# Kernel optimization log

Hardware: AMD Instinct MI355X
Metric: run time of the kernel (lower is better)

Reference implementation:

```python
import jax, jax.numpy as jnp
import numpy as np

N = 20000
E = 160000
H = 8          # heads
D = 96         # head_dim (768 // 8)
C = H * D      # 768 hidden channels
G = 256        # num graphs
NUM_CLASSES = 32
SLOPE = 0.2    # GATv2 LeakyReLU negative slope


def layer_norm(x, w, b, eps=1e-5):
    mu = jnp.mean(x, axis=-1, keepdims=True)
    var = jnp.mean(jnp.square(x - mu), axis=-1, keepdims=True)
    return (x - mu) * jax.lax.rsqrt(var + eps) * w + b


def gatv2_layer(x, src, dst, Wl, bl, Wr, br, att, bias):
    # x: [N, C]; src/dst: [E'] with self loops included
    xl = (x @ Wl + bl).reshape(N, H, D)   # source projection
    xr = (x @ Wr + br).reshape(N, H, D)   # target projection
    e = xl[src] + xr[dst]                 # [E', H, D] edge gather
    e = jnp.where(e > 0, e, SLOPE * e)    # LeakyReLU
    logits = jnp.einsum('ehd,hd->eh', e, att)  # [E', H]
    m = jax.ops.segment_max(logits, dst, num_segments=N)
    ex = jnp.exp(logits - m[dst])
    s = jax.ops.segment_sum(ex, dst, num_segments=N)
    alpha = ex / s[dst]                   # segment softmax over in-edges
    out = jax.ops.segment_sum(alpha[:, :, None] * xl[src], dst, num_segments=N)
    return out.reshape(N, C) + bias


def setup_inputs() -> dict:
    key = jax.random.key(0)
    ks = jax.random.split(key, 24)
    x = jax.random.normal(ks[0], (N, 768), jnp.float32)
    edge_index = jax.random.randint(ks[1], (2, E), 0, N, jnp.int64)
    batch = jnp.sort(jax.random.randint(ks[2], (N,), 0, G, jnp.int64))
    sc = 1.0 / np.sqrt(C)
    p = {
        'x': x, 'edge_index': edge_index, 'batch': batch,
        'w_in': jax.random.normal(ks[3], (768, C), jnp.float32) * sc,
        'b_in': jnp.zeros((C,), jnp.float32),
        'Wl': jax.random.normal(ks[4], (3, C, C), jnp.float32) * sc,
        'bl': jnp.zeros((3, C), jnp.float32),
        'Wr': jax.random.normal(ks[5], (3, C, C), jnp.float32) * sc,
        'br': jnp.zeros((3, C), jnp.float32),
        'att': jax.random.normal(ks[6], (3, H, D), jnp.float32) * (1.0 / np.sqrt(D)),
        'gat_bias': jnp.zeros((3, C), jnp.float32),
        'ln_w': jnp.ones((3, C), jnp.float32),
        'ln_b': jnp.zeros((3, C), jnp.float32),
        'out_ln_w': jnp.ones((3 * C,), jnp.float32),
        'out_ln_b': jnp.zeros((3 * C,), jnp.float32),
        'w_out': jax.random.normal(ks[7], (3 * C, NUM_CLASSES), jnp.float32) * (1.0 / np.sqrt(3 * C)),
        'b_out': jnp.zeros((NUM_CLASSES,), jnp.float32),
    }
    return p


def reference(x, edge_index, batch, w_in, b_in, Wl, bl, Wr, br, att, gat_bias,
              ln_w, ln_b, out_ln_w, out_ln_b, w_out, b_out):
    # add self loops (PyG add_self_loops=True)
    loops = jnp.arange(N, dtype=edge_index.dtype)
    src = jnp.concatenate([edge_index[0], loops])
    dst = jnp.concatenate([edge_index[1], loops])

    h = x @ w_in + b_in
    jumps = []
    for l in range(3):
        a = gatv2_layer(h, src, dst, Wl[l], bl[l], Wr[l], br[l], att[l], gat_bias[l])
        h = layer_norm(a + h, ln_w[l], ln_b[l])
        h = jax.nn.gelu(h, approximate=False)
        jumps.append(h)
    hc = jnp.concatenate(jumps, axis=-1)  # JumpingKnowledge 'cat' -> [N, 3C]

    # global mean pool over graphs
    sums = jax.ops.segment_sum(hc, batch, num_segments=G)
    cnt = jax.ops.segment_sum(jnp.ones((N, 1), hc.dtype), batch, num_segments=G)
    pooled = sums / jnp.maximum(cnt, 1.0)

    out = layer_norm(pooled, out_ln_w, out_ln_b)
    return out @ w_out + b_out
```

## Files before the change

### kernel.cpp

```cpp
#include <hip/hip_runtime.h>

#define N_NODES 20000
#define N_EDGES 160000
#define CH      768
#define CH3     2304
#define NGRAPH  256
#define NCLS    32

typedef __bf16 bf16v8 __attribute__((ext_vector_type(8)));
typedef float  f32x4  __attribute__((ext_vector_type(4)));

__device__ __forceinline__ float b2f(ushort u) {
    union { float f; unsigned u; } x; x.u = ((unsigned)u) << 16; return x.f;
}
__device__ __forceinline__ ushort f2b(float f) {
    union { float f; unsigned u; } x; x.f = f;
    unsigned r = x.u + 0x7FFFu + ((x.u >> 16) & 1u);
    return (ushort)(r >> 16);
}
__device__ __forceinline__ void load12(const ushort* __restrict__ p, float* o) {
    const ushort4* q = (const ushort4*)p;
    ushort4 a = q[0], b = q[1], c = q[2];
    o[0]=b2f(a.x); o[1]=b2f(a.y); o[2]=b2f(a.z); o[3]=b2f(a.w);
    o[4]=b2f(b.x); o[5]=b2f(b.y); o[6]=b2f(b.z); o[7]=b2f(b.w);
    o[8]=b2f(c.x); o[9]=b2f(c.y); o[10]=b2f(c.z); o[11]=b2f(c.w);
}
__device__ __forceinline__ void load12f(const float* __restrict__ p, float* o) {
    const float4* q = (const float4*)p;
    float4 a = q[0], b = q[1], c = q[2];
    o[0]=a.x; o[1]=a.y; o[2]=a.z; o[3]=a.w;
    o[4]=b.x; o[5]=b.y; o[6]=b.z; o[7]=b.w;
    o[8]=c.x; o[9]=c.y; o[10]=c.z; o[11]=c.w;
}
__device__ __forceinline__ void async_copy16(void* lds, const void* gp) {
    __builtin_amdgcn_global_load_lds((const void __attribute__((address_space(1)))*)gp,
                                     (void __attribute__((address_space(3)))*)lds, 16, 0, 0);
}

__global__ void cvt_x_kernel(const float* __restrict__ src, ushort* __restrict__ dst, int n4) {
    int i = blockIdx.x * 256 + threadIdx.x;
    if (i >= n4) return;
    float4 v = ((const float4*)src)[i];
    ushort4 o; o.x = f2b(v.x); o.y = f2b(v.y); o.z = f2b(v.z); o.w = f2b(v.w);
    ((ushort4*)dst)[i] = o;
}

__global__ void transpose_cvt_all(const float* __restrict__ w_in,
                                  const float* __restrict__ Wl,
                                  const float* __restrict__ Wr,
                                  ushort* __restrict__ wt_in,
                                  ushort* __restrict__ wt_l) {
    __shared__ float tile[32][33];
    int z = blockIdx.z;
    const float* in;
    ushort* out;
    if (z == 0) { in = w_in; out = wt_in; }
    else {
        int l = (z - 1) >> 1, isr = (z - 1) & 1;
        in  = (isr ? Wr : Wl) + (size_t)l * CH * CH;
        out = wt_l + (size_t)l * 1536 * CH + (size_t)isr * CH * CH;
    }
    int bx = blockIdx.x * 32, by = blockIdx.y * 32;
    int tx = threadIdx.x, ty = threadIdx.y;
    #pragma unroll
    for (int i = ty; i < 32; i += 8) tile[i][tx] = in[(size_t)(by + i) * CH + bx + tx];
    __syncthreads();
    #pragma unroll
    for (int i = ty; i < 32; i += 8) out[(size_t)(bx + i) * CH + by + tx] = f2b(tile[tx][i]);
}

__global__ void init_kernel(int* deg, int* gcount, int n) {
    int i = blockIdx.x * 256 + threadIdx.x;
    if (i < n) deg[i] = 1;
    if (i < 256) gcount[i] = 0;
}
__global__ void count_both_kernel(const int* __restrict__ dst, int* __restrict__ deg, int e,
                                  const int* __restrict__ batch, int* __restrict__ gcount, int n) {
    int i = blockIdx.x * 256 + threadIdx.x;
    if (i < e) atomicAdd(&deg[dst[i]], 1);
    if (i < n) atomicAdd(&gcount[batch[i]], 1);
}
__global__ __launch_bounds__(1024) void scan_kernel(const int* __restrict__ deg,
                                                    int* __restrict__ rowptr, int n) {
    __shared__ int part[1024];
    int t = threadIdx.x;
    const int chunk = (n + 1023) / 1024;
    int base = t * chunk;
    int s = 0;
    for (int i = 0; i < chunk; ++i) { int idx = base + i; if (idx < n) s += deg[idx]; }
    part[t] = s; __syncthreads();
    for (int off = 1; off < 1024; off <<= 1) {
        int v = (t >= off) ? part[t - off] : 0;
        __syncthreads();
        part[t] += v;
        __syncthreads();
    }
    int run = (t == 0) ? 0 : part[t - 1];
    for (int i = 0; i < chunk; ++i) {
        int idx = base + i;
        if (idx < n) { rowptr[idx] = run; run += deg[idx]; }
    }
    if (t == 1023) rowptr[n] = part[1023];
}
__global__ void selfloop_kernel(const int* __restrict__ rowptr, int* __restrict__ csrc,
                                int* __restrict__ cursor, int n) {
    int i = blockIdx.x * 256 + threadIdx.x;
    if (i < n) { int p = rowptr[i]; csrc[p] = i; cursor[i] = p + 1; }
}
__global__ void scatter_kernel(const int* __restrict__ src, const int* __restrict__ dst,
                               int* __restrict__ cursor, int* __restrict__ csrc, int e) {
    int i = blockIdx.x * 256 + threadIdx.x;
    if (i < e) { int p = atomicAdd(&cursor[dst[i]], 1); csrc[p] = src[i]; }
}
__global__ __launch_bounds__(256) void gscan_kernel(const int* __restrict__ gcount,
                                                    int* __restrict__ gstart) {
    __shared__ int p[256];
    int t = threadIdx.x;
    p[t] = gcount[t]; __syncthreads();
    for (int off = 1; off < 256; off <<= 1) {
        int v = (t >= off) ? p[t - off] : 0;
        __syncthreads();
        p[t] += v;
        __syncthreads();
    }
    gstart[t] = p[t] - gcount[t];
    if (t == 255) gstart[256] = p[255];
}

__global__ __launch_bounds__(256) void gemm_bf16_kernel(
    const ushort* __restrict__ A, int lda,
    const ushort* __restrict__ Bt,
    const float* __restrict__ biasA, const float* __restrict__ biasB, int nsplit,
    ushort* __restrict__ C, int ldc, int M) {
    __shared__ __bf16 As[128 * 32];
    __shared__ __bf16 Bs[128 * 32];
    int tid = threadIdx.x;
    int wave = tid >> 6, lane = tid & 63;
    int wr = wave >> 1, wc = wave & 1;

    int bid = blockIdx.y * gridDim.x + blockIdx.x;
    int pf = 8 * gridDim.y;
    int p  = bid / pf;
    int rem = bid - p * pf;
    int rp = min(8, (int)gridDim.x - p * 8);
    int row_t = p * 8 + rem % rp;
    int col_t = rem / rp;
    int row0 = row_t * 128, col0 = col_t * 128;

    int c1 = wave * 64 + lane, c2 = c1 + 256;
    int ar1 = min(row0 + (c1 >> 2), M - 1), ak1 = (c1 & 3) * 8;
    int ar2 = min(row0 + (c2 >> 2), M - 1), ak2 = (c2 & 3) * 8;
    int br1 = col0 + (c1 >> 2), br2 = col0 + (c2 >> 2);
    const ushort* a1 = A + (size_t)ar1 * lda + ak1;
    const ushort* a2 = A + (size_t)ar2 * lda + ak2;
    const ushort* b1 = Bt + (size_t)br1 * CH + ak1;
    const ushort* b2 = Bt + (size_t)br2 * CH + ak2;
    __bf16* asb1 = As + (wave * 64) * 8;
    __bf16* asb2 = As + (256 + wave * 64) * 8;
    __bf16* bsb1 = Bs + (wave * 64) * 8;
    __bf16* bsb2 = Bs + (256 + wave * 64) * 8;

    f32x4 acc[4][4] = {};
    int l16 = lane & 15, lq = lane >> 4;

    for (int k0 = 0; k0 < CH; k0 += 32) {
        async_copy16(asb1, a1 + k0);
        async_copy16(asb2, a2 + k0);
        async_copy16(bsb1, b1 + k0);
        async_copy16(bsb2, b2 + k0);
        __syncthreads();
        bf16v8 av[4], bv[4];
        #pragma unroll
        for (int i = 0; i < 4; ++i)
            av[i] = *(const bf16v8*)(As + ((wr * 64 + i * 16 + l16) * 32 + lq * 8));
        #pragma unroll
        for (int j = 0; j < 4; ++j)
            bv[j] = *(const bf16v8*)(Bs + ((wc * 64 + j * 16 + l16) * 32 + lq * 8));
        #pragma unroll
        for (int i = 0; i < 4; ++i)
            #pragma unroll
            for (int j = 0; j < 4; ++j)
                acc[i][j] = __builtin_amdgcn_mfma_f32_16x16x32_bf16(av[i], bv[j], acc[i][j], 0, 0, 0);
        __syncthreads();
    }
    #pragma unroll
    for (int i = 0; i < 4; ++i) {
        int mbase = row0 + wr * 64 + i * 16 + lq * 4;
        #pragma unroll
        for (int j = 0; j < 4; ++j) {
            int col = col0 + wc * 64 + j * 16 + l16;
            float bb = (col < nsplit) ? biasA[col] : biasB[col - nsplit];
            #pragma unroll
            for (int r = 0; r < 4; ++r) {
                int mm = mbase + r;
                if (mm < M) C[(size_t)mm * ldc + col] = f2b(acc[i][j][r] + bb);
            }
        }
    }
}

__global__ __launch_bounds__(256) void gat_node_kernel(
    const ushort* __restrict__ xlxr,
    const ushort* __restrict__ hin, int ldh,
    const int* __restrict__ rowptr, const int* __restrict__ csrc,
    const float* __restrict__ att, const float* __restrict__ gbias,
    const float* __restrict__ lnw, const float* __restrict__ lnb,
    ushort* __restrict__ hout, int nn) {
    int wv = threadIdx.x >> 6, lane = threadIdx.x & 63;
    int n = blockIdx.x * 4 + wv;
    if (n >= nn) return;
    int c0 = lane * 12;
    float attv[12], xr[12], acc1[12], acc2[12];
    load12f(att + c0, attv);
    load12(xlxr + (size_t)n * 1536 + CH + c0, xr);
    #pragma unroll
    for (int j = 0; j < 12; ++j) { acc1[j] = 0.f; acc2[j] = 0.f; }
    float m1 = -1e30f, s1 = 0.f, m2 = -1e30f, s2 = 0.f;
    int rs = rowptr[n], re = rowptr[n + 1];
    int e = rs;
    for (; e + 1 < re; e += 2) {
        int sa = csrc[e], sb = csrc[e + 1];
        float xa[12], xb[12];
        load12(xlxr + (size_t)sa * 1536 + c0, xa);
        load12(xlxr + (size_t)sb * 1536 + c0, xb);
        float da = 0.f, db = 0.f;
        #pragma unroll
        for (int j = 0; j < 12; ++j) {
            float va = xa[j] + xr[j]; va = (va > 0.f) ? va : 0.2f * va;
            float vb = xb[j] + xr[j]; vb = (vb > 0.f) ? vb : 0.2f * vb;
            da = fmaf(va, attv[j], da);
            db = fmaf(vb, attv[j], db);
        }
        da += __shfl_xor(da, 1); db += __shfl_xor(db, 1);
        da += __shfl_xor(da, 2); db += __shfl_xor(db, 2);
        da += __shfl_xor(da, 4); db += __shfl_xor(db, 4);
        float nm1 = fmaxf(m1, da), nm2 = fmaxf(m2, db);
        float sc1 = __expf(m1 - nm1), sc2 = __expf(m2 - nm2);
        float ex1 = __expf(da - nm1), ex2 = __expf(db - nm2);
        s1 = s1 * sc1 + ex1;
        s2 = s2 * sc2 + ex2;
        #pragma unroll
        for (int j = 0; j < 12; ++j) {
            acc1[j] = fmaf(acc1[j], sc1, ex1 * xa[j]);
            acc2[j] = fmaf(acc2[j], sc2, ex2 * xb[j]);
        }
        m1 = nm1; m2 = nm2;
    }
    if (e < re) {
        int sa = csrc[e];
        float xa[12];
        load12(xlxr + (size_t)sa * 1536 + c0, xa);
        float da = 0.f;
        #pragma unroll
        for (int j = 0; j < 12; ++j) {
            float va = xa[j] + xr[j]; va = (va > 0.f) ? va : 0.2f * va;
            da = fmaf(va, attv[j], da);
        }
        da += __shfl_xor(da, 1);
        da += __shfl_xor(da, 2);
        da += __shfl_xor(da, 4);
        float nm = fmaxf(m1, da);
        float sc = __expf(m1 - nm), ex = __expf(da - nm);
        s1 = s1 * sc + ex;
        #pragma unroll
        for (int j = 0; j < 12; ++j) acc1[j] = fmaf(acc1[j], sc, ex * xa[j]);
        m1 = nm;
    }
    float M = fmaxf(m1, m2);
    float w1 = __expf(m1 - M), w2 = __expf(m2 - M);
    float ssum = s1 * w1 + s2 * w2;
    float inv = 1.f / ssum;
    float hres[12], gb[12], tv[12];
    load12(hin + (size_t)n * ldh + c0, hres);
    load12f(gbias + c0, gb);
    float lsum = 0.f;
    #pragma unroll
    for (int j = 0; j < 12; ++j) {
        tv[j] = (acc1[j] * w1 + acc2[j] * w2) * inv + gb[j] + hres[j];
        lsum += tv[j];
    }
    #pragma unroll
    for (int o = 1; o < 64; o <<= 1) lsum += __shfl_xor(lsum, o);
    float mu = lsum * (1.f / 768.f);
    float lsq = 0.f;
    #pragma unroll
    for (int j = 0; j < 12; ++j) { float d = tv[j] - mu; lsq = fmaf(d, d, lsq); }
    #pragma unroll
    for (int o = 1; o < 64; o <<= 1) lsq += __shfl_xor(lsq, o);
    float rstd = rsqrtf(lsq * (1.f / 768.f) + 1e-5f);
    float wv12[12], bv12[12];
    load12f(lnw + c0, wv12);
    load12f(lnb + c0, bv12);
    ushort* op = hout + (size_t)n * CH3 + c0;
    #pragma unroll
    for (int j = 0; j < 12; ++j) {
        float y = (tv[j] - mu) * rstd * wv12[j] + bv12[j];
        float g = 0.5f * y * (1.f + erff(y * 0.70710678118f));
        op[j] = f2b(g);
    }
}

__global__ __launch_bounds__(256) void pool_kernel(const ushort* __restrict__ hc,
                                                   const int* __restrict__ gstart,
                                                   float* __restrict__ pooled) {
    int g = blockIdx.x;
    int c = blockIdx.y * 256 + threadIdx.x;
    int s = gstart[g], e = gstart[g + 1];
    const ushort* p = hc + (size_t)s * CH3 + c;
    float a = 0.f;
    for (int n = s; n < e; ++n) { a += b2f(*p); p += CH3; }
    pooled[(size_t)g * CH3 + c] = a * (1.f / (float)max(e - s, 1));
}

__global__ __launch_bounds__(256) void head_kernel(const float* __restrict__ pooled,
                                                   const float* __restrict__ olnw,
                                                   const float* __restrict__ olnb,
                                                   const float* __restrict__ wout,
                                                   const float* __restrict__ bout,
                                                   float* __restrict__ outp) {
    __shared__ float row[CH3];
    __shared__ float red[8];
    __shared__ float parts[8][32];
    int g = blockIdx.x, t = threadIdx.x;
    int lane = t & 63, wv = t >> 6;
    float s = 0.f;
    for (int c = t; c < CH3; c += 256) { float v = pooled[(size_t)g * CH3 + c]; row[c] = v; s += v; }
    #pragma unroll
    for (int o = 1; o < 64; o <<= 1) s += __shfl_xor(s, o);
    if (lane == 0) red[wv] = s;
    __syncthreads();
    float mu = (red[0] + red[1] + red[2] + red[3]) * (1.f / (float)CH3);
    float q = 0.f;
    for (int c = t; c < CH3; c += 256) { float d = row[c] - mu; q += d * d; }
    #pragma unroll
    for (int o = 1; o < 64; o <<= 1) q += __shfl_xor(q, o);
    if (lane == 0) red[4 + wv] = q;
    __syncthreads();
    float rstd = rsqrtf((red[4] + red[5] + red[6] + red[7]) * (1.f / (float)CH3) + 1e-5f);
    for (int c = t; c < CH3; c += 256)
        row[c] = (row[c] - mu) * rstd * olnw[c] + olnb[c];
    __syncthreads();
    int j = t & 31, slice = t >> 5;
    float a = 0.f;
    int cb = slice * (CH3 / 8);
    for (int c = cb; c < cb + CH3 / 8; ++c) a += row[c] * wout[(size_t)c * 32 + j];
    parts[slice][j] = a;
    __syncthreads();
    if (t < 32) {
        float r = bout[t];
        #pragma unroll
        for (int si = 0; si < 8; ++si) r += parts[si][t];
        outp[(size_t)g * 32 + t] = r;
    }
}

extern "C" void kernel_launch(void* const* d_in, const int* in_sizes, int n_in,
                              void* d_out, int out_size, void* d_ws, size_t ws_size,
                              hipStream_t stream) {
    const float* x     = (const float*)d_in[0];
    const int*   ei    = (const int*)d_in[1];
    const int*   batch = (const int*)d_in[2];
    const float* w_in  = (const float*)d_in[3];
    const float* b_in  = (const float*)d_in[4];
    const float* Wl    = (const float*)d_in[5];
    const float* bl    = (const float*)d_in[6];
    const float* Wr    = (const float*)d_in[7];
    const float* br    = (const float*)d_in[8];
    const float* att   = (const float*)d_in[9];
    const float* gbias = (const float*)d_in[10];
    const float* lnw   = (const float*)d_in[11];
    const float* lnb   = (const float*)d_in[12];
    const float* olnw  = (const float*)d_in[13];
    const float* olnb  = (const float*)d_in[14];
    const float* wout  = (const float*)d_in[15];
    const float* bout  = (const float*)d_in[16];

    char* ws = (char*)d_ws;
    size_t off = 0;
    auto alloc = [&](size_t bytes) -> void* {
        void* p = ws + off;
        off = (off + bytes + 255) & ~(size_t)255;
        return p;
    };
    ushort* h0     = (ushort*)alloc((size_t)N_NODES * CH * 2);
    ushort* hc     = (ushort*)alloc((size_t)N_NODES * CH3 * 2);
    ushort* xlxr   = (ushort*)alloc((size_t)N_NODES * 1536 * 2);
    ushort* wt_in  = (ushort*)alloc((size_t)CH * CH * 2);
    ushort* wt_l   = (ushort*)alloc((size_t)3 * 1536 * CH * 2);
    int*    deg    = (int*)alloc((size_t)N_NODES * 4);
    int*    rowptr = (int*)alloc((size_t)(N_NODES + 1) * 4);
    int*    cursor = (int*)alloc((size_t)N_NODES * 4);
    int*    csrc   = (int*)alloc((size_t)(N_EDGES + N_NODES) * 4);
    int*    gcount = (int*)alloc(256 * 4);
    int*    gstart = (int*)alloc(257 * 4);
    float*  pooled = (float*)alloc((size_t)NGRAPH * CH3 * 4);
    if (off > ws_size) return;

    ushort* xc = hc;

    cvt_x_kernel<<<(N_NODES * CH / 4 + 255) / 256, 256, 0, stream>>>(x, xc, N_NODES * CH / 4);
    transpose_cvt_all<<<dim3(24, 24, 7), dim3(32, 8), 0, stream>>>(w_in, Wl, Wr, wt_in, wt_l);

    int nb = (N_NODES + 255) / 256, eb = (N_EDGES + 255) / 256;
    init_kernel<<<nb, 256, 0, stream>>>(deg, gcount, N_NODES);
    count_both_kernel<<<eb, 256, 0, stream>>>(ei + N_EDGES, deg, N_EDGES, batch, gcount, N_NODES);
    scan_kernel<<<1, 1024, 0, stream>>>(deg, rowptr, N_NODES);
    selfloop_kernel<<<nb, 256, 0, stream>>>(rowptr, csrc, cursor, N_NODES);
    scatter_kernel<<<eb, 256, 0, stream>>>(ei, ei + N_EDGES, cursor, csrc, N_EDGES);
    gscan_kernel<<<1, 256, 0, stream>>>(gcount, gstart);

    gemm_bf16_kernel<<<dim3(157, 6), 256, 0, stream>>>(
        xc, CH, wt_in, b_in, b_in, CH, h0, CH, N_NODES);

    for (int l = 0; l < 3; ++l) {
        const ushort* hprev = (l == 0) ? h0 : (hc + (size_t)(l - 1) * CH);
        int ldh = (l == 0) ? CH : CH3;
        gemm_bf16_kernel<<<dim3(157, 12), 256, 0, stream>>>(
            hprev, ldh, wt_l + (size_t)l * 1536 * CH,
            bl + (size_t)l * CH, br + (size_t)l * CH, CH,
            xlxr, 1536, N_NODES);
        gat_node_kernel<<<N_NODES / 4, 256, 0, stream>>>(
            xlxr, hprev, ldh, rowptr, csrc,
            att + (size_t)l * CH, gbias + (size_t)l * CH,
            lnw + (size_t)l * CH, lnb + (size_t)l * CH,
            hc + (size_t)l * CH, N_NODES);
    }

    pool_kernel<<<dim3(NGRAPH, CH3 / 256), 256, 0, stream>>>(hc, gstart, pooled);
    head_kernel<<<NGRAPH, 256, 0, stream>>>(pooled, olnw, olnb, wout, bout, (float*)d_out);
}
```

Baseline: 754.3 us.

## Drop online-max softmax, single-pass layernorm stats, vectorized stores, unrolled pooling

```diff
diff --git a/kernel.cpp b/kernel.cpp
--- a/kernel.cpp
+++ b/kernel.cpp
@@ -69,16 +69,11 @@
     for (int i = ty; i < 32; i += 8) out[(size_t)(bx + i) * CH + by + tx] = f2b(tile[tx][i]);
 }
 
-__global__ void init_kernel(int* deg, int* gcount, int n) {
-    int i = blockIdx.x * 256 + threadIdx.x;
-    if (i < n) deg[i] = 1;
-    if (i < 256) gcount[i] = 0;
-}
 __global__ void count_both_kernel(const int* __restrict__ dst, int* __restrict__ deg, int e,
                                   const int* __restrict__ batch, int* __restrict__ gcount, int n) {
     int i = blockIdx.x * 256 + threadIdx.x;
     if (i < e) atomicAdd(&deg[dst[i]], 1);
-    if (i < n) atomicAdd(&gcount[batch[i]], 1);
+    if (i < n) { atomicAdd(&deg[i], 1); atomicAdd(&gcount[batch[i]], 1); }
 }
 __global__ __launch_bounds__(1024) void scan_kernel(const int* __restrict__ deg,
                                                     int* __restrict__ rowptr, int n) {
@@ -208,95 +203,88 @@
     ushort* __restrict__ hout, int nn) {
     int wv = threadIdx.x >> 6, lane = threadIdx.x & 63;
     int n = blockIdx.x * 4 + wv;
-    if (n >= nn) return;
     int c0 = lane * 12;
-    float attv[12], xr[12], acc1[12], acc2[12];
+    const ushort* __restrict__ xbase = xlxr + c0;
+    float attv[12], xr[12], acc1[12] = {}, acc2[12] = {};
     load12f(att + c0, attv);
-    load12(xlxr + (size_t)n * 1536 + CH + c0, xr);
-    #pragma unroll
-    for (int j = 0; j < 12; ++j) { acc1[j] = 0.f; acc2[j] = 0.f; }
-    float m1 = -1e30f, s1 = 0.f, m2 = -1e30f, s2 = 0.f;
+    load12(xbase + (size_t)n * 1536 + CH, xr);
+    float s1 = 0.f, s2 = 0.f;
     int rs = rowptr[n], re = rowptr[n + 1];
     int e = rs;
     for (; e + 1 < re; e += 2) {
         int sa = csrc[e], sb = csrc[e + 1];
         float xa[12], xb[12];
-        load12(xlxr + (size_t)sa * 1536 + c0, xa);
-        load12(xlxr + (size_t)sb * 1536 + c0, xb);
+        load12(xbase + (size_t)sa * 1536, xa);
+        load12(xbase + (size_t)sb * 1536, xb);
         float da = 0.f, db = 0.f;
         #pragma unroll
         for (int j = 0; j < 12; ++j) {
-            float va = xa[j] + xr[j]; va = (va > 0.f) ? va : 0.2f * va;
-            float vb = xb[j] + xr[j]; vb = (vb > 0.f) ? vb : 0.2f * vb;
+            float va = xa[j] + xr[j]; va = fmaxf(va, 0.2f * va);
+            float vb = xb[j] + xr[j]; vb = fmaxf(vb, 0.2f * vb);
             da = fmaf(va, attv[j], da);
             db = fmaf(vb, attv[j], db);
         }
         da += __shfl_xor(da, 1); db += __shfl_xor(db, 1);
         da += __shfl_xor(da, 2); db += __shfl_xor(db, 2);
         da += __shfl_xor(da, 4); db += __shfl_xor(db, 4);
-        float nm1 = fmaxf(m1, da), nm2 = fmaxf(m2, db);
-        float sc1 = __expf(m1 - nm1), sc2 = __expf(m2 - nm2);
-        float ex1 = __expf(da - nm1), ex2 = __expf(db - nm2);
-        s1 = s1 * sc1 + ex1;
-        s2 = s2 * sc2 + ex2;
+        float ea = __expf(da), eb = __expf(db);
+        s1 += ea; s2 += eb;
         #pragma unroll
         for (int j = 0; j < 12; ++j) {
-            acc1[j] = fmaf(acc1[j], sc1, ex1 * xa[j]);
-            acc2[j] = fmaf(acc2[j], sc2, ex2 * xb[j]);
+            acc1[j] = fmaf(ea, xa[j], acc1[j]);
+            acc2[j] = fmaf(eb, xb[j], acc2[j]);
         }
-        m1 = nm1; m2 = nm2;
     }
     if (e < re) {
         int sa = csrc[e];
         float xa[12];
-        load12(xlxr + (size_t)sa * 1536 + c0, xa);
+        load12(xbase + (size_t)sa * 1536, xa);
         float da = 0.f;
         #pragma unroll
         for (int j = 0; j < 12; ++j) {
-            float va = xa[j] + xr[j]; va = (va > 0.f) ? va : 0.2f * va;
+            float va = xa[j] + xr[j]; va = fmaxf(va, 0.2f * va);
             da = fmaf(va, attv[j], da);
         }
         da += __shfl_xor(da, 1);
         da += __shfl_xor(da, 2);
         da += __shfl_xor(da, 4);
-        float nm = fmaxf(m1, da);
-        float sc = __expf(m1 - nm), ex = __expf(da - nm);
-        s1 = s1 * sc + ex;
-        #pragma unroll
-        for (int j = 0; j < 12; ++j) acc1[j] = fmaf(acc1[j], sc, ex * xa[j]);
-        m1 = nm;
-    }
-    float M = fmaxf(m1, m2);
-    float w1 = __expf(m1 - M), w2 = __expf(m2 - M);
-    float ssum = s1 * w1 + s2 * w2;
-    float inv = 1.f / ssum;
+        float ea = __expf(da);
+        s1 += ea;
+        #pragma unroll
+        for (int j = 0; j < 12; ++j) acc1[j] = fmaf(ea, xa[j], acc1[j]);
+    }
+    float inv = 1.f / (s1 + s2);
     float hres[12], gb[12], tv[12];
     load12(hin + (size_t)n * ldh + c0, hres);
     load12f(gbias + c0, gb);
-    float lsum = 0.f;
+    float lsum = 0.f, lsq = 0.f;
     #pragma unroll
     for (int j = 0; j < 12; ++j) {
-        tv[j] = (acc1[j] * w1 + acc2[j] * w2) * inv + gb[j] + hres[j];
+        tv[j] = (acc1[j] + acc2[j]) * inv + gb[j] + hres[j];
         lsum += tv[j];
-    }
-    #pragma unroll
-    for (int o = 1; o < 64; o <<= 1) lsum += __shfl_xor(lsum, o);
+        lsq = fmaf(tv[j], tv[j], lsq);
+    }
+    #pragma unroll
+    for (int o = 1; o < 64; o <<= 1) { lsum += __shfl_xor(lsum, o); lsq += __shfl_xor(lsq, o); }
     float mu = lsum * (1.f / 768.f);
-    float lsq = 0.f;
-    #pragma unroll
-    for (int j = 0; j < 12; ++j) { float d = tv[j] - mu; lsq = fmaf(d, d, lsq); }
-    #pragma unroll
-    for (int o = 1; o < 64; o <<= 1) lsq += __shfl_xor(lsq, o);
-    float rstd = rsqrtf(lsq * (1.f / 768.f) + 1e-5f);
+    float var = lsq * (1.f / 768.f) - mu * mu;
+    float rstd = rsqrtf(var + 1e-5f);
     float wv12[12], bv12[12];
     load12f(lnw + c0, wv12);
     load12f(lnb + c0, bv12);
     ushort* op = hout + (size_t)n * CH3 + c0;
-    #pragma unroll
-    for (int j = 0; j < 12; ++j) {
-        float y = (tv[j] - mu) * rstd * wv12[j] + bv12[j];
-        float g = 0.5f * y * (1.f + erff(y * 0.70710678118f));
-        op[j] = f2b(g);
+    ushort4 u[3];
+    #pragma unroll
+    for (int k = 0; k < 3; ++k) {
+        float g[4];
+        #pragma unroll
+        for (int q = 0; q < 4; ++q) {
+            int j = k * 4 + q;
+            float y = (tv[j] - mu) * rstd * wv12[j] + bv12[j];
+            g[q] = 0.5f * y * (1.f + erff(y * 0.70710678118f));
+        }
+        u[k].x = f2b(g[0]); u[k].y = f2b(g[1]); u[k].z = f2b(g[2]); u[k].w = f2b(g[3]);
+        ((ushort4*)op)[k] = u[k];
     }
 }
 
@@ -307,8 +295,17 @@
     int c = blockIdx.y * 256 + threadIdx.x;
     int s = gstart[g], e = gstart[g + 1];
     const ushort* p = hc + (size_t)s * CH3 + c;
-    float a = 0.f;
-    for (int n = s; n < e; ++n) { a += b2f(*p); p += CH3; }
+    float a0 = 0.f, a1 = 0.f, a2 = 0.f, a3 = 0.f;
+    int n = s;
+    for (; n + 3 < e; n += 4) {
+        a0 += b2f(p[0]);
+        a1 += b2f(p[CH3]);
+        a2 += b2f(p[2 * CH3]);
+        a3 += b2f(p[3 * CH3]);
+        p += 4 * CH3;
+    }
+    for (; n < e; ++n) { a0 += b2f(*p); p += CH3; }
+    float a = (a0 + a1) + (a2 + a3);
     pooled[(size_t)g * CH3 + c] = a * (1.f / (float)max(e - s, 1));
 }
 
@@ -402,7 +399,8 @@
     transpose_cvt_all<<<dim3(24, 24, 7), dim3(32, 8), 0, stream>>>(w_in, Wl, Wr, wt_in, wt_l);
 
     int nb = (N_NODES + 255) / 256, eb = (N_EDGES + 255) / 256;
-    init_kernel<<<nb, 256, 0, stream>>>(deg, gcount, N_NODES);
+    hipMemsetAsync(deg, 0, (size_t)N_NODES * 4, stream);
+    hipMemsetAsync(gcount, 0, 256 * 4, stream);
     count_both_kernel<<<eb, 256, 0, stream>>>(ei + N_EDGES, deg, N_EDGES, batch, gcount, N_NODES);
     scan_kernel<<<1, 1024, 0, stream>>>(deg, rowptr, N_NODES);
     selfloop_kernel<<<nb, 256, 0, stream>>>(rowptr, csrc, cursor, N_NODES);
```

Result: faster. 712.4 us (-5.6%).
